# Kernel optimization log

Hardware: AMD Instinct MI355X
Metric: run time of the kernel (lower is better)

Reference implementation:

```python
import jax, jax.numpy as jnp
import numpy as np
import math

EMBED_DIM = 1024
NUM_HEADS = 16
HEAD_DIM = EMBED_DIM // NUM_HEADS
D_FF = 4 * EMBED_DIM
EPS = 1e-6  # flax LayerNorm default


def _layer_norm(x, scale, bias):
    mu = jnp.mean(x, axis=-1, keepdims=True)
    var = jnp.mean(jnp.square(x - mu), axis=-1, keepdims=True)
    return (x - mu) * jax.lax.rsqrt(var + EPS) * scale + bias


def setup_inputs() -> dict:
    key = jax.random.key(0)
    ks = jax.random.split(key, 12)
    B, T, D = 8, 1024, EMBED_DIM
    x = jax.random.normal(ks[0], (B, T, D), dtype=jnp.float32)
    # causal mask broadcastable to [B, H, T, T]
    mask = jnp.tril(jnp.ones((T, T), dtype=bool))[None, None, :, :]
    mask = jnp.broadcast_to(mask, (B, 1, T, T))
    s = 0.02
    return {
        "x": x,
        "mask": mask,
        "ln1_scale": jnp.ones((D,), jnp.float32),
        "ln1_bias": jnp.zeros((D,), jnp.float32),
        "wq": jax.random.normal(ks[1], (D, D), jnp.float32) * s,
        "bq": jnp.zeros((D,), jnp.float32),
        "wk": jax.random.normal(ks[2], (D, D), jnp.float32) * s,
        "bk": jnp.zeros((D,), jnp.float32),
        "wv": jax.random.normal(ks[3], (D, D), jnp.float32) * s,
        "bv": jnp.zeros((D,), jnp.float32),
        "wo": jax.random.normal(ks[4], (D, D), jnp.float32) * s,
        "bo": jnp.zeros((D,), jnp.float32),
        "ln2_scale": jnp.ones((D,), jnp.float32),
        "ln2_bias": jnp.zeros((D,), jnp.float32),
        "w1": jax.random.normal(ks[5], (D, D_FF), jnp.float32) * s,
        "b1": jnp.zeros((D_FF,), jnp.float32),
        "w2": jax.random.normal(ks[6], (D_FF, D), jnp.float32) * s,
        "b2": jnp.zeros((D,), jnp.float32),
    }


def reference(x, mask, ln1_scale, ln1_bias, wq, bq, wk, bk, wv, bv, wo, bo,
              ln2_scale, ln2_bias, w1, b1, w2, b2):
    B, T, D = x.shape
    residual = x
    h = _layer_norm(x, ln1_scale, ln1_bias)
    q = (h @ wq + bq).reshape(B, T, NUM_HEADS, HEAD_DIM)
    k = (h @ wk + bk).reshape(B, T, NUM_HEADS, HEAD_DIM)
    v = (h @ wv + bv).reshape(B, T, NUM_HEADS, HEAD_DIM)
    # scores: [B, H, T, T]
    scores = jnp.einsum("bqhd,bkhd->bhqk", q, k) / math.sqrt(HEAD_DIM)
    scores = jnp.where(mask, scores, -1e9)
    probs = jax.nn.softmax(scores, axis=-1)
    # dropout is identity (deterministic=True)
    out = jnp.einsum("bhqk,bkhd->bqhd", probs, v).reshape(B, T, D)
    h = out @ wo + bo
    x = h + residual
    residual = x
    h = _layer_norm(x, ln2_scale, ln2_bias)
    h = jax.nn.gelu(h @ w1 + b1, approximate=True)  # flax nn.gelu default
    h = h @ w2 + b2
    return h + residual
```

## Files before the change

kernel.cpp:

```cpp
#include <hip/hip_runtime.h>
#include <hip/hip_bf16.h>

using bf16 = __hip_bfloat16;
typedef __attribute__((ext_vector_type(8))) short bf16x8;
typedef __attribute__((ext_vector_type(4))) float f32x4;

__device__ inline float u2f(unsigned int u) { return __uint_as_float(u << 16); }
__device__ inline float toF(float x) { return x; }
__device__ inline float toF(bf16 x) { return __bfloat162float(x); }
__device__ inline void storeO(float* p, float v) { *p = v; }
__device__ inline void storeO(bf16* p, float v) { *p = __float2bfloat16(v); }

__device__ inline void gload_lds16(const void* g, void* l) {
    __builtin_amdgcn_global_load_lds(
        (const __attribute__((address_space(1))) void*)g,
        (__attribute__((address_space(3))) void*)l, 16, 0, 0);
}

__device__ inline void wgbar() {
    asm volatile("s_waitcnt lgkmcnt(0)" ::: "memory");
    __builtin_amdgcn_s_barrier();
    asm volatile("" ::: "memory");
}

__device__ inline int swzb(int row, int bcol) {
    return row * 128 + (bcol ^ (((row ^ (row >> 3)) & 7) << 4));
}

__global__ __launch_bounds__(256) void transpose_k(const float* __restrict__ in,
                                                   bf16* __restrict__ out,
                                                   int R, int C) {
    __shared__ float tile[32][33];
    const int c0 = blockIdx.x * 32, r0 = blockIdx.y * 32;
    const int tx = threadIdx.x & 31, ty = threadIdx.x >> 5;
#pragma unroll
    for (int i = 0; i < 32; i += 8)
        tile[ty + i][tx] = in[(size_t)(r0 + ty + i) * C + (c0 + tx)];
    __syncthreads();
#pragma unroll
    for (int i = 0; i < 32; i += 8)
        out[(size_t)(c0 + ty + i) * R + (r0 + tx)] = __float2bfloat16(tile[tx][ty + i]);
}

__global__ __launch_bounds__(256) void catb_k(const float* __restrict__ a,
                                              const float* __restrict__ b,
                                              const float* __restrict__ c,
                                              float* __restrict__ o) {
    const int t = blockIdx.x * 256 + threadIdx.x;
    const float* s = t < 1024 ? a : (t < 2048 ? b : c);
    o[t] = s[t & 1023];
}

__device__ inline float waveRedSum(float x) {
#pragma unroll
    for (int off = 32; off; off >>= 1) x += __shfl_xor(x, off, 64);
    return x;
}

template <typename T>
__global__ __launch_bounds__(256) void layernorm_k(const T* __restrict__ in,
                                                   const float* __restrict__ g,
                                                   const float* __restrict__ bta,
                                                   bf16* __restrict__ out) {
    const int row = blockIdx.x, t = threadIdx.x;
    const int lane = t & 63, wid = t >> 6;
    const T* xr = in + (size_t)row * 1024;
    float v0, v1, v2, v3;
    if constexpr (sizeof(T) == 4) {
        float4 u = ((const float4*)xr)[t];
        v0 = u.x; v1 = u.y; v2 = u.z; v3 = u.w;
    } else {
        ushort4 u = ((const ushort4*)xr)[t];
        v0 = u2f(u.x); v1 = u2f(u.y); v2 = u2f(u.z); v3 = u2f(u.w);
    }
    __shared__ float red[8];
    float s = waveRedSum(v0 + v1 + v2 + v3);
    if (lane == 0) red[wid] = s;
    __syncthreads();
    float mu = (red[0] + red[1] + red[2] + red[3]) * (1.f / 1024.f);
    float d0 = v0 - mu, d1 = v1 - mu, d2 = v2 - mu, d3 = v3 - mu;
    float ss = waveRedSum(d0 * d0 + d1 * d1 + d2 * d2 + d3 * d3);
    if (lane == 0) red[4 + wid] = ss;
    __syncthreads();
    float var = (red[4] + red[5] + red[6] + red[7]) * (1.f / 1024.f);
    float inv = rsqrtf(var + 1e-6f);
    const int c = t * 4;
    bf16* orow = out + (size_t)row * 1024;
    orow[c + 0] = __float2bfloat16(d0 * inv * g[c + 0] + bta[c + 0]);
    orow[c + 1] = __float2bfloat16(d1 * inv * g[c + 1] + bta[c + 1]);
    orow[c + 2] = __float2bfloat16(d2 * inv * g[c + 2] + bta[c + 2]);
    orow[c + 3] = __float2bfloat16(d3 * inv * g[c + 3] + bta[c + 3]);
}

template <int GELU, int RES, int ACC, typename RT, typename OT>
__global__ __launch_bounds__(256) void mgemm_k(const bf16* __restrict__ A,
                                               const bf16* __restrict__ B, int ldB,
                                               const float* __restrict__ bias,
                                               const RT* __restrict__ resid,
                                               OT* C, int M, int N, int K, int gx) {
    __shared__ bf16 As[2 * 128 * 32];
    __shared__ bf16 Bs[2 * 128 * 32];
    const int tid = threadIdx.x;
    const int lane = tid & 63, wid = tid >> 6;
    const int l16 = lane & 15, quad = lane >> 4;
    const int wm = (wid >> 1) * 64, wn = (wid & 1) * 64;
    const int nwg = gridDim.x;
    const int wg = ((blockIdx.x & 7) * (nwg >> 3)) + (blockIdx.x >> 3);
    const int m0 = (wg / gx) * 128, n0 = (wg % gx) * 128;

    const int r0 = tid >> 2, sc0 = tid & 3;
    const int lc0 = sc0 ^ ((r0 >> 1) & 3);
    const int r1 = r0 + 64;
    const int lc1 = sc0 ^ ((r1 >> 1) & 3);
    const bf16* gA0 = A + (size_t)(m0 + r0) * K + lc0 * 8;
    const bf16* gA1 = A + (size_t)(m0 + r1) * K + lc1 * 8;
    const bf16* gB0 = B + (size_t)(n0 + r0) * ldB + lc0 * 8;
    const bf16* gB1 = B + (size_t)(n0 + r1) * ldB + lc1 * 8;
    char* asb = (char*)As;
    char* bsb = (char*)Bs;
    const int lb0 = wid * 1024, lb1 = 4096 + wid * 1024;
    const int rdsw = (quad ^ ((l16 >> 1) & 3)) * 16;

    f32x4 acc[4][4] = {};
    const int nT = K >> 5;
    gload_lds16(gA0, asb + lb0);
    gload_lds16(gA1, asb + lb1);
    gload_lds16(gB0, bsb + lb0);
    gload_lds16(gB1, bsb + lb1);
    __syncthreads();
    for (int t = 0; t < nT; ++t) {
        const int cur = t & 1;
        if (t + 1 < nT) {
            char* ab = asb + (cur ^ 1) * 8192;
            char* bb = bsb + (cur ^ 1) * 8192;
            const int ko = (t + 1) * 32;
            gload_lds16(gA0 + ko, ab + lb0);
            gload_lds16(gA1 + ko, ab + lb1);
            gload_lds16(gB0 + ko, bb + lb0);
            gload_lds16(gB1 + ko, bb + lb1);
        }
        const char* ar = asb + cur * 8192;
        const char* br = bsb + cur * 8192;
        bf16x8 a[4], b[4];
#pragma unroll
        for (int i = 0; i < 4; ++i)
            a[i] = *(const bf16x8*)(ar + (wm + i * 16 + l16) * 64 + rdsw);
#pragma unroll
        for (int i = 0; i < 4; ++i)
            b[i] = *(const bf16x8*)(br + (wn + i * 16 + l16) * 64 + rdsw);
        __builtin_amdgcn_s_setprio(1);
#pragma unroll
        for (int mi = 0; mi < 4; ++mi)
#pragma unroll
            for (int ni = 0; ni < 4; ++ni)
                acc[mi][ni] = __builtin_amdgcn_mfma_f32_16x16x32_bf16(
                    a[mi], b[ni], acc[mi][ni], 0, 0, 0);
        __builtin_amdgcn_s_setprio(0);
        __syncthreads();
    }
#pragma unroll
    for (int mi = 0; mi < 4; ++mi) {
#pragma unroll
        for (int ni = 0; ni < 4; ++ni) {
            const int col = n0 + wn + ni * 16 + l16;
            const float bv = bias ? bias[col] : 0.f;
#pragma unroll
            for (int r = 0; r < 4; ++r) {
                const int row = m0 + wm + mi * 16 + quad * 4 + r;
                float val = acc[mi][ni][r] + bv;
                if (GELU) {
                    float z = 0.7978845608028654f * (val + 0.044715f * val * val * val);
                    float th = 1.f - 2.f / (__expf(2.f * z) + 1.f);
                    val = 0.5f * val * (1.f + th);
                }
                const size_t idx = (size_t)row * N + col;
                if (RES) val += toF(resid[idx]);
                if (ACC) val += toF(C[idx]);
                storeO(&C[idx], val);
            }
        }
    }
}

__global__ __launch_bounds__(256) void attn_k(const bf16* __restrict__ q,
                                              const bf16* __restrict__ k,
                                              const bf16* __restrict__ v,
                                              bf16* __restrict__ o, int rs) {
    const int bid = blockIdx.x;
    const int u = bid & 255, top = bid >> 8;
    const int xx = u & 3;
    const int h = (u >> 2) & 15;
    const int b = top * 4 + (u >> 6);
    const int qi = top ? 3 - xx : xx;
    const int qblock = qi * 256;
    const int tid = threadIdx.x;
    const int wave = tid >> 6, lane = tid & 63;
    const int l16 = lane & 15, quad = lane >> 4;
    const int q0w = qblock + wave * 64;

    __shared__ __align__(16) bf16 Kl[64 * 64];
    __shared__ __align__(16) bf16 Vt[64 * 64];
    __shared__ __align__(16) bf16 Pl[4 * 64 * 64];
    __shared__ __align__(16) float sc[4][64];

    bf16x8 qf[4][2];
#pragma unroll
    for (int ni = 0; ni < 4; ++ni) {
        const int row = q0w + ni * 16 + l16;
        const bf16* qp = q + ((size_t)b * 1024 + row) * rs + h * 64;
#pragma unroll
        for (int kc = 0; kc < 2; ++kc)
            qf[ni][kc] = *(const bf16x8*)(qp + kc * 32 + quad * 8);
    }

    f32x4 acc[4][4] = {};
    float mrun[4], lrun[4];
#pragma unroll
    for (int ni = 0; ni < 4; ++ni) { mrun[ni] = -1e30f; lrun[ni] = 0.f; }

    const int NT = qi * 4 + 4;
    const int myNT = qi * 4 + wave + 1;

    const int kr_ = tid >> 3, kch = tid & 7;
    const int vr_ = (tid >> 3) * 2, vdb = (tid & 7) * 8;
    uint4 kA, kB, vA, vB;
    {
        const size_t gk = ((size_t)b * 1024 + 0 + kr_) * rs + h * 64 + kch * 8;
        kA = *(const uint4*)(k + gk);
        kB = *(const uint4*)(k + gk + (size_t)32 * rs);
        const size_t gv = ((size_t)b * 1024 + 0 + vr_) * rs + h * 64 + vdb;
        vA = *(const uint4*)(v + gv);
        vB = *(const uint4*)(v + gv + rs);
    }

    for (int t = 0; t < NT; ++t) {
        wgbar();
        *(uint4*)((char*)Kl + swzb(kr_, kch * 16)) = kA;
        *(uint4*)((char*)Kl + swzb(kr_ + 32, kch * 16)) = kB;
        {
            const unsigned aw[4] = {vA.x, vA.y, vA.z, vA.w};
            const unsigned bw[4] = {vB.x, vB.y, vB.z, vB.w};
#pragma unroll
            for (int j = 0; j < 8; ++j) {
                const unsigned lo = (aw[j >> 1] >> ((j & 1) * 16)) & 0xffffu;
                const unsigned hi = (bw[j >> 1] >> ((j & 1) * 16)) & 0xffffu;
                *(unsigned*)((char*)Vt + swzb(vdb + j, vr_ * 2)) = lo | (hi << 16);
            }
        }
        if (t + 1 < NT) {
            const int j1 = (t + 1) * 64;
            const size_t gk = ((size_t)b * 1024 + j1 + kr_) * rs + h * 64 + kch * 8;
            kA = *(const uint4*)(k + gk);
            kB = *(const uint4*)(k + gk + (size_t)32 * rs);
            const size_t gv = ((size_t)b * 1024 + j1 + vr_) * rs + h * 64 + vdb;
            vA = *(const uint4*)(v + gv);
            vB = *(const uint4*)(v + gv + rs);
        }
        wgbar();
        if (t < myNT) {
            const int j0 = t * 64;
            f32x4 st[4][4] = {};
#pragma unroll
            for (int kc = 0; kc < 2; ++kc) {
                bf16x8 kf[4];
#pragma unroll
                for (int mi = 0; mi < 4; ++mi)
                    kf[mi] = *(const bf16x8*)((char*)Kl +
                             swzb(mi * 16 + l16, kc * 64 + quad * 16));
                __builtin_amdgcn_s_setprio(1);
#pragma unroll
                for (int mi = 0; mi < 4; ++mi)
#pragma unroll
                    for (int ni = 0; ni < 4; ++ni)
                        st[mi][ni] = __builtin_amdgcn_mfma_f32_16x16x32_bf16(
                            kf[mi], qf[ni][kc], st[mi][ni], 0, 0, 0);
                __builtin_amdgcn_s_setprio(0);
            }
            if (j0 == q0w) {
#pragma unroll
                for (int mi = 0; mi < 4; ++mi)
#pragma unroll
                    for (int ni = 0; ni < 4; ++ni)
#pragma unroll
                        for (int r = 0; r < 4; ++r)
                            if (mi * 16 + quad * 4 + r > ni * 16 + l16)
                                st[mi][ni][r] = -1e30f;
            }
            float mx[4];
#pragma unroll
            for (int ni = 0; ni < 4; ++ni) {
                float a0 = fmaxf(st[0][ni][0], st[0][ni][1]);
                float a1 = fmaxf(st[0][ni][2], st[0][ni][3]);
                float a2 = fmaxf(st[1][ni][0], st[1][ni][1]);
                float a3 = fmaxf(st[1][ni][2], st[1][ni][3]);
                float a4 = fmaxf(st[2][ni][0], st[2][ni][1]);
                float a5 = fmaxf(st[2][ni][2], st[2][ni][3]);
                float a6 = fmaxf(st[3][ni][0], st[3][ni][1]);
                float a7 = fmaxf(st[3][ni][2], st[3][ni][3]);
                float m_ = fmaxf(fmaxf(fmaxf(a0, a1), fmaxf(a2, a3)),
                                 fmaxf(fmaxf(a4, a5), fmaxf(a6, a7)));
                m_ = fmaxf(m_, __shfl_xor(m_, 16, 64));
                m_ = fmaxf(m_, __shfl_xor(m_, 32, 64));
                mx[ni] = m_;
            }
            const bool need = (mx[0] > mrun[0] + 64.f) | (mx[1] > mrun[1] + 64.f) |
                              (mx[2] > mrun[2] + 64.f) | (mx[3] > mrun[3] + 64.f);
            if (__any(need)) {
                float fac[4];
#pragma unroll
                for (int ni = 0; ni < 4; ++ni) {
                    const float nm = (mx[ni] > mrun[ni] + 64.f) ? mx[ni] : mrun[ni];
                    fac[ni] = __expf((mrun[ni] - nm) * 0.125f);
                    mrun[ni] = nm;
                    lrun[ni] *= fac[ni];
                }
                if (quad == 0)
#pragma unroll
                    for (int ni = 0; ni < 4; ++ni) sc[wave][ni * 16 + l16] = fac[ni];
#pragma unroll
                for (int mi = 0; mi < 4; ++mi) {
                    const f32x4 f4 = *(const f32x4*)&sc[wave][mi * 16 + quad * 4];
#pragma unroll
                    for (int ni = 0; ni < 4; ++ni)
#pragma unroll
                        for (int r = 0; r < 4; ++r) acc[mi][ni][r] *= f4[r];
                }
            }
#pragma unroll
            for (int ni = 0; ni < 4; ++ni) {
                const float mm = mrun[ni];
                float t0 = 0.f, t1 = 0.f, t2 = 0.f, t3 = 0.f;
#pragma unroll
                for (int mi = 0; mi < 4; ++mi) {
                    float p0 = __expf((st[mi][ni][0] - mm) * 0.125f);
                    float p1 = __expf((st[mi][ni][1] - mm) * 0.125f);
                    float p2 = __expf((st[mi][ni][2] - mm) * 0.125f);
                    float p3 = __expf((st[mi][ni][3] - mm) * 0.125f);
                    st[mi][ni][0] = p0; st[mi][ni][1] = p1;
                    st[mi][ni][2] = p2; st[mi][ni][3] = p3;
                    t0 += p0; t1 += p1; t2 += p2; t3 += p3;
                }
                float ls = (t0 + t1) + (t2 + t3);
                ls += __shfl_xor(ls, 16, 64);
                ls += __shfl_xor(ls, 32, 64);
                lrun[ni] += ls;
            }
            char* Pb = (char*)Pl + wave * 8192;
#pragma unroll
            for (int ni = 0; ni < 4; ++ni) {
                const int qrow = ni * 16 + l16;
#pragma unroll
                for (int mi = 0; mi < 4; ++mi) {
                    union { bf16 bv[4]; uint2 u2; } pk;
#pragma unroll
                    for (int r = 0; r < 4; ++r)
                        pk.bv[r] = __float2bfloat16(st[mi][ni][r]);
                    *(uint2*)(Pb + swzb(qrow, mi * 32 + quad * 8)) = pk.u2;
                }
            }
#pragma unroll
            for (int kc = 0; kc < 2; ++kc) {
                bf16x8 pf[4], vf[4];
#pragma unroll
                for (int mi = 0; mi < 4; ++mi)
                    pf[mi] = *(const bf16x8*)(Pb +
                             swzb(mi * 16 + l16, kc * 64 + quad * 16));
#pragma unroll
                for (int ni = 0; ni < 4; ++ni)
                    vf[ni] = *(const bf16x8*)((char*)Vt +
                             swzb(ni * 16 + l16, kc * 64 + quad * 16));
                __builtin_amdgcn_s_setprio(1);
#pragma unroll
                for (int mi = 0; mi < 4; ++mi)
#pragma unroll
                    for (int ni = 0; ni < 4; ++ni)
                        acc[mi][ni] = __builtin_amdgcn_mfma_f32_16x16x32_bf16(
                            pf[mi], vf[ni], acc[mi][ni], 0, 0, 0);
                __builtin_amdgcn_s_setprio(0);
            }
        }
    }
    if (quad == 0)
#pragma unroll
        for (int ni = 0; ni < 4; ++ni) sc[wave][ni * 16 + l16] = lrun[ni];
#pragma unroll
    for (int mi = 0; mi < 4; ++mi) {
        const f32x4 l4 = *(const f32x4*)&sc[wave][mi * 16 + quad * 4];
#pragma unroll
        for (int r = 0; r < 4; ++r) {
            const float inv = 1.f / l4[r];
            const int row = q0w + mi * 16 + quad * 4 + r;
            bf16* orow = o + ((size_t)b * 1024 + row) * 1024 + h * 64;
#pragma unroll
            for (int ni = 0; ni < 4; ++ni)
                orow[ni * 16 + l16] = __float2bfloat16(acc[mi][ni][r] * inv);
        }
    }
}

extern "C" void kernel_launch(void* const* d_in, const int* in_sizes, int n_in,
                              void* d_out, int out_size, void* d_ws, size_t ws_size,
                              hipStream_t stream) {
    (void)out_size; (void)ws_size;
    const float* x = (const float*)d_in[0];
    const int base = (n_in >= 18 && in_sizes[1] > 4096) ? 2 : 1;
    const float* ln1s = (const float*)d_in[base + 0];
    const float* ln1b = (const float*)d_in[base + 1];
    const float* wq   = (const float*)d_in[base + 2];
    const float* bq   = (const float*)d_in[base + 3];
    const float* wk   = (const float*)d_in[base + 4];
    const float* bk   = (const float*)d_in[base + 5];
    const float* wv   = (const float*)d_in[base + 6];
    const float* bv   = (const float*)d_in[base + 7];
    const float* wo   = (const float*)d_in[base + 8];
    const float* bo   = (const float*)d_in[base + 9];
    const float* ln2s = (const float*)d_in[base + 10];
    const float* ln2b = (const float*)d_in[base + 11];
    const float* w1   = (const float*)d_in[base + 12];
    const float* b1   = (const float*)d_in[base + 13];
    const float* w2   = (const float*)d_in[base + 14];
    const float* b2   = (const float*)d_in[base + 15];
    float* out = (float*)d_out;

    char* ws = (char*)d_ws;
    char* oc = (char*)d_out;
    const size_t MB = 1ull << 20;
    bf16* h     = (bf16*)(ws + 0 * MB);
    bf16* qkv   = (bf16*)(ws + 16 * MB);
    bf16* ao    = (bf16*)(ws + 0 * MB);
    bf16* h2    = (bf16*)(ws + 0 * MB);
    bf16* woT   = (bf16*)(ws + 16 * MB);
    bf16* f1c   = (bf16*)(ws + 16 * MB);
    bf16* w1T   = (bf16*)(ws + 48 * MB);
    bf16* w2T   = (bf16*)(ws + 56 * MB);
    bf16* wqkvT = (bf16*)(oc + 0 * MB);
    float* bqkv = (float*)(oc + 8 * MB);

    const dim3 tb(256);

    layernorm_k<float><<<8192, tb, 0, stream>>>(x, ln1s, ln1b, h);
    transpose_k<<<dim3(32, 32), tb, 0, stream>>>(wq, wqkvT, 1024, 1024);
    transpose_k<<<dim3(32, 32), tb, 0, stream>>>(wk, wqkvT + 1024 * 1024, 1024, 1024);
    transpose_k<<<dim3(32, 32), tb, 0, stream>>>(wv, wqkvT + 2 * 1024 * 1024, 1024, 1024);
    catb_k<<<12, tb, 0, stream>>>(bq, bk, bv, bqkv);
    mgemm_k<0, 0, 0, float, bf16><<<1536, tb, 0, stream>>>(
        h, wqkvT, 1024, bqkv, nullptr, qkv, 8192, 3072, 1024, 24);
    attn_k<<<512, tb, 0, stream>>>(qkv, qkv + 1024, qkv + 2048, ao, 3072);
    transpose_k<<<dim3(32, 32), tb, 0, stream>>>(wo, woT, 1024, 1024);
    transpose_k<<<dim3(128, 32), tb, 0, stream>>>(w1, w1T, 1024, 4096);
    transpose_k<<<dim3(32, 128), tb, 0, stream>>>(w2, w2T, 4096, 1024);
    mgemm_k<0, 1, 0, float, float><<<512, tb, 0, stream>>>(
        ao, woT, 1024, bo, x, out, 8192, 1024, 1024, 8);
    layernorm_k<float><<<8192, tb, 0, stream>>>(out, ln2s, ln2b, h2);
    for (int c = 0; c < 2; ++c) {
        mgemm_k<1, 0, 0, float, bf16><<<1024, tb, 0, stream>>>(
            h2, w1T + (size_t)c * 2048 * 1024, 1024, b1 + c * 2048, nullptr,
            f1c, 8192, 2048, 1024, 16);
        mgemm_k<0, 0, 1, float, float><<<512, tb, 0, stream>>>(
            f1c, w2T + c * 2048, 4096, c ? nullptr : b2, nullptr,
            out, 8192, 1024, 2048, 8);
    }
}
```

Before: 584.3 us.

## Triple-buffer GEMM loads and add 256x256 tile kernel for QKV and FFN1

```diff
diff --git a/kernel.cpp b/kernel.cpp
--- a/kernel.cpp
+++ b/kernel.cpp
@@ -98,8 +98,8 @@
                                                const float* __restrict__ bias,
                                                const RT* __restrict__ resid,
                                                OT* C, int M, int N, int K, int gx) {
-    __shared__ bf16 As[2 * 128 * 32];
-    __shared__ bf16 Bs[2 * 128 * 32];
+    __shared__ bf16 As[3 * 128 * 32];
+    __shared__ bf16 Bs[3 * 128 * 32];
     const int tid = threadIdx.x;
     const int lane = tid & 63, wid = tid >> 6;
     const int l16 = lane & 15, quad = lane >> 4;
@@ -123,24 +123,35 @@
 
     f32x4 acc[4][4] = {};
     const int nT = K >> 5;
-    gload_lds16(gA0, asb + lb0);
-    gload_lds16(gA1, asb + lb1);
-    gload_lds16(gB0, bsb + lb0);
-    gload_lds16(gB1, bsb + lb1);
-    __syncthreads();
+#pragma unroll
+    for (int p = 0; p < 2; ++p) {
+        char* ab = asb + p * 8192;
+        char* bb = bsb + p * 8192;
+        const int ko = p * 32;
+        gload_lds16(gA0 + ko, ab + lb0);
+        gload_lds16(gA1 + ko, ab + lb1);
+        gload_lds16(gB0 + ko, bb + lb0);
+        gload_lds16(gB1 + ko, bb + lb1);
+    }
+    int issued = 2;
     for (int t = 0; t < nT; ++t) {
-        const int cur = t & 1;
-        if (t + 1 < nT) {
-            char* ab = asb + (cur ^ 1) * 8192;
-            char* bb = bsb + (cur ^ 1) * 8192;
-            const int ko = (t + 1) * 32;
+        if (issued > t + 1)
+            asm volatile("s_waitcnt vmcnt(4)" ::: "memory");
+        else
+            asm volatile("s_waitcnt vmcnt(0)" ::: "memory");
+        __builtin_amdgcn_s_barrier();
+        if (issued < nT) {
+            char* ab = asb + (issued % 3) * 8192;
+            char* bb = bsb + (issued % 3) * 8192;
+            const int ko = issued * 32;
             gload_lds16(gA0 + ko, ab + lb0);
             gload_lds16(gA1 + ko, ab + lb1);
             gload_lds16(gB0 + ko, bb + lb0);
             gload_lds16(gB1 + ko, bb + lb1);
-        }
-        const char* ar = asb + cur * 8192;
-        const char* br = bsb + cur * 8192;
+            ++issued;
+        }
+        const char* ar = asb + (t % 3) * 8192;
+        const char* br = bsb + (t % 3) * 8192;
         bf16x8 a[4], b[4];
 #pragma unroll
         for (int i = 0; i < 4; ++i)
@@ -156,7 +167,6 @@
                 acc[mi][ni] = __builtin_amdgcn_mfma_f32_16x16x32_bf16(
                     a[mi], b[ni], acc[mi][ni], 0, 0, 0);
         __builtin_amdgcn_s_setprio(0);
-        __syncthreads();
     }
 #pragma unroll
     for (int mi = 0; mi < 4; ++mi) {
@@ -177,6 +187,103 @@
                 if (RES) val += toF(resid[idx]);
                 if (ACC) val += toF(C[idx]);
                 storeO(&C[idx], val);
+            }
+        }
+    }
+}
+
+template <int GELU>
+__global__ __launch_bounds__(512, 2) void gemm256_k(const bf16* __restrict__ A,
+                                                    const bf16* __restrict__ B, int ldB,
+                                                    const float* __restrict__ bias,
+                                                    bf16* __restrict__ C,
+                                                    int M, int N, int K, int gx) {
+    __shared__ bf16 As[3 * 256 * 32];
+    __shared__ bf16 Bs[3 * 256 * 32];
+    const int tid = threadIdx.x;
+    const int lane = tid & 63, wid = tid >> 6;
+    const int l16 = lane & 15, quad = lane >> 4;
+    const int wm = (wid >> 2) * 128, wn = (wid & 3) * 64;
+    const int nwg = gridDim.x;
+    const int wg = ((blockIdx.x & 7) * (nwg >> 3)) + (blockIdx.x >> 3);
+    const int m0 = (wg / gx) * 256, n0 = (wg % gx) * 256;
+
+    const int r0 = tid >> 2, sc0 = tid & 3;
+    const int lc0 = sc0 ^ ((r0 >> 1) & 3);
+    const int r1 = r0 + 128;
+    const int lc1 = sc0 ^ ((r1 >> 1) & 3);
+    const bf16* gA0 = A + (size_t)(m0 + r0) * K + lc0 * 8;
+    const bf16* gA1 = A + (size_t)(m0 + r1) * K + lc1 * 8;
+    const bf16* gB0 = B + (size_t)(n0 + r0) * ldB + lc0 * 8;
+    const bf16* gB1 = B + (size_t)(n0 + r1) * ldB + lc1 * 8;
+    char* asb = (char*)As;
+    char* bsb = (char*)Bs;
+    const int lb0 = wid * 1024, lb1 = 8192 + wid * 1024;
+    const int rdsw = (quad ^ ((l16 >> 1) & 3)) * 16;
+
+    f32x4 acc[8][4] = {};
+    const int nT = K >> 5;
+#pragma unroll
+    for (int p = 0; p < 2; ++p) {
+        char* ab = asb + p * 16384;
+        char* bb = bsb + p * 16384;
+        const int ko = p * 32;
+        gload_lds16(gA0 + ko, ab + lb0);
+        gload_lds16(gA1 + ko, ab + lb1);
+        gload_lds16(gB0 + ko, bb + lb0);
+        gload_lds16(gB1 + ko, bb + lb1);
+    }
+    int issued = 2;
+    for (int t = 0; t < nT; ++t) {
+        if (issued > t + 1)
+            asm volatile("s_waitcnt vmcnt(4)" ::: "memory");
+        else
+            asm volatile("s_waitcnt vmcnt(0)" ::: "memory");
+        __builtin_amdgcn_s_barrier();
+        if (issued < nT) {
+            char* ab = asb + (issued % 3) * 16384;
+            char* bb = bsb + (issued % 3) * 16384;
+            const int ko = issued * 32;
+            gload_lds16(gA0 + ko, ab + lb0);
+            gload_lds16(gA1 + ko, ab + lb1);
+            gload_lds16(gB0 + ko, bb + lb0);
+            gload_lds16(gB1 + ko, bb + lb1);
+            ++issued;
+        }
+        const char* ar = asb + (t % 3) * 16384;
+        const char* br = bsb + (t % 3) * 16384;
+        bf16x8 a[8], b[4];
+#pragma unroll
+        for (int i = 0; i < 8; ++i)
+            a[i] = *(const bf16x8*)(ar + (wm + i * 16 + l16) * 64 + rdsw);
+#pragma unroll
+        for (int i = 0; i < 4; ++i)
+            b[i] = *(const bf16x8*)(br + (wn + i * 16 + l16) * 64 + rdsw);
+        __builtin_amdgcn_s_setprio(1);
+#pragma unroll
+        for (int mi = 0; mi < 8; ++mi)
+#pragma unroll
+            for (int ni = 0; ni < 4; ++ni)
+                acc[mi][ni] = __builtin_amdgcn_mfma_f32_16x16x32_bf16(
+                    a[mi], b[ni], acc[mi][ni], 0, 0, 0);
+        __builtin_amdgcn_s_setprio(0);
+    }
+#pragma unroll
+    for (int mi = 0; mi < 8; ++mi) {
+#pragma unroll
+        for (int ni = 0; ni < 4; ++ni) {
+            const int col = n0 + wn + ni * 16 + l16;
+            const float bv = bias[col];
+#pragma unroll
+            for (int r = 0; r < 4; ++r) {
+                const int row = m0 + wm + mi * 16 + quad * 4 + r;
+                float val = acc[mi][ni][r] + bv;
+                if (GELU) {
+                    float z = 0.7978845608028654f * (val + 0.044715f * val * val * val);
+                    float th = 1.f - 2.f / (__expf(2.f * z) + 1.f);
+                    val = 0.5f * val * (1.f + th);
+                }
+                C[(size_t)row * N + col] = __float2bfloat16(val);
             }
         }
     }
@@ -443,8 +550,8 @@
     transpose_k<<<dim3(32, 32), tb, 0, stream>>>(wk, wqkvT + 1024 * 1024, 1024, 1024);
     transpose_k<<<dim3(32, 32), tb, 0, stream>>>(wv, wqkvT + 2 * 1024 * 1024, 1024, 1024);
     catb_k<<<12, tb, 0, stream>>>(bq, bk, bv, bqkv);
-    mgemm_k<0, 0, 0, float, bf16><<<1536, tb, 0, stream>>>(
-        h, wqkvT, 1024, bqkv, nullptr, qkv, 8192, 3072, 1024, 24);
+    gemm256_k<0><<<384, 512, 0, stream>>>(
+        h, wqkvT, 1024, bqkv, qkv, 8192, 3072, 1024, 12);
     attn_k<<<512, tb, 0, stream>>>(qkv, qkv + 1024, qkv + 2048, ao, 3072);
     transpose_k<<<dim3(32, 32), tb, 0, stream>>>(wo, woT, 1024, 1024);
     transpose_k<<<dim3(128, 32), tb, 0, stream>>>(w1, w1T, 1024, 4096);
@@ -453,9 +560,9 @@
         ao, woT, 1024, bo, x, out, 8192, 1024, 1024, 8);
     layernorm_k<float><<<8192, tb, 0, stream>>>(out, ln2s, ln2b, h2);
     for (int c = 0; c < 2; ++c) {
-        mgemm_k<1, 0, 0, float, bf16><<<1024, tb, 0, stream>>>(
-            h2, w1T + (size_t)c * 2048 * 1024, 1024, b1 + c * 2048, nullptr,
-            f1c, 8192, 2048, 1024, 16);
+        gemm256_k<1><<<256, 512, 0, stream>>>(
+            h2, w1T + (size_t)c * 2048 * 1024, 1024, b1 + c * 2048,
+            f1c, 8192, 2048, 1024, 8);
         mgemm_k<0, 0, 1, float, float><<<512, tb, 0, stream>>>(
             f1c, w2T + c * 2048, 4096, c ? nullptr : b2, nullptr,
             out, 8192, 1024, 2048, 8);
```

After: 602.3 us. 3.1% more time.

## Triple-buffer GEMM LDS loads with vmcnt waits and merge QKV weight transposes

Applied to the files above, without the earlier changes.

```diff
diff --git a/kernel.cpp b/kernel.cpp
--- a/kernel.cpp
+++ b/kernel.cpp
@@ -40,6 +40,24 @@
 #pragma unroll
     for (int i = 0; i < 32; i += 8)
         out[(size_t)(c0 + ty + i) * R + (r0 + tx)] = __float2bfloat16(tile[tx][ty + i]);
+}
+
+__global__ __launch_bounds__(256) void qkvT_k(const float* __restrict__ wq,
+                                              const float* __restrict__ wk,
+                                              const float* __restrict__ wv,
+                                              bf16* __restrict__ out) {
+    __shared__ float tile[32][33];
+    const float* in = blockIdx.z == 0 ? wq : (blockIdx.z == 1 ? wk : wv);
+    bf16* o = out + (size_t)blockIdx.z * 1024 * 1024;
+    const int c0 = blockIdx.x * 32, r0 = blockIdx.y * 32;
+    const int tx = threadIdx.x & 31, ty = threadIdx.x >> 5;
+#pragma unroll
+    for (int i = 0; i < 32; i += 8)
+        tile[ty + i][tx] = in[(size_t)(r0 + ty + i) * 1024 + (c0 + tx)];
+    __syncthreads();
+#pragma unroll
+    for (int i = 0; i < 32; i += 8)
+        o[(size_t)(c0 + ty + i) * 1024 + (r0 + tx)] = __float2bfloat16(tile[tx][ty + i]);
 }
 
 __global__ __launch_bounds__(256) void catb_k(const float* __restrict__ a,
@@ -98,8 +116,8 @@
                                                const float* __restrict__ bias,
                                                const RT* __restrict__ resid,
                                                OT* C, int M, int N, int K, int gx) {
-    __shared__ bf16 As[2 * 128 * 32];
-    __shared__ bf16 Bs[2 * 128 * 32];
+    __shared__ bf16 As[3 * 128 * 32];
+    __shared__ bf16 Bs[3 * 128 * 32];
     const int tid = threadIdx.x;
     const int lane = tid & 63, wid = tid >> 6;
     const int l16 = lane & 15, quad = lane >> 4;
@@ -123,24 +141,35 @@
 
     f32x4 acc[4][4] = {};
     const int nT = K >> 5;
-    gload_lds16(gA0, asb + lb0);
-    gload_lds16(gA1, asb + lb1);
-    gload_lds16(gB0, bsb + lb0);
-    gload_lds16(gB1, bsb + lb1);
-    __syncthreads();
+#pragma unroll
+    for (int p = 0; p < 2; ++p) {
+        char* ab = asb + p * 8192;
+        char* bb = bsb + p * 8192;
+        const int ko = p * 32;
+        gload_lds16(gA0 + ko, ab + lb0);
+        gload_lds16(gA1 + ko, ab + lb1);
+        gload_lds16(gB0 + ko, bb + lb0);
+        gload_lds16(gB1 + ko, bb + lb1);
+    }
+    int issued = 2;
     for (int t = 0; t < nT; ++t) {
-        const int cur = t & 1;
-        if (t + 1 < nT) {
-            char* ab = asb + (cur ^ 1) * 8192;
-            char* bb = bsb + (cur ^ 1) * 8192;
-            const int ko = (t + 1) * 32;
+        if (issued > t + 1)
+            asm volatile("s_waitcnt vmcnt(4)" ::: "memory");
+        else
+            asm volatile("s_waitcnt vmcnt(0)" ::: "memory");
+        __builtin_amdgcn_s_barrier();
+        if (issued < nT) {
+            char* ab = asb + (issued % 3) * 8192;
+            char* bb = bsb + (issued % 3) * 8192;
+            const int ko = issued * 32;
             gload_lds16(gA0 + ko, ab + lb0);
             gload_lds16(gA1 + ko, ab + lb1);
             gload_lds16(gB0 + ko, bb + lb0);
             gload_lds16(gB1 + ko, bb + lb1);
-        }
-        const char* ar = asb + cur * 8192;
-        const char* br = bsb + cur * 8192;
+            ++issued;
+        }
+        const char* ar = asb + (t % 3) * 8192;
+        const char* br = bsb + (t % 3) * 8192;
         bf16x8 a[4], b[4];
 #pragma unroll
         for (int i = 0; i < 4; ++i)
@@ -156,7 +185,6 @@
                 acc[mi][ni] = __builtin_amdgcn_mfma_f32_16x16x32_bf16(
                     a[mi], b[ni], acc[mi][ni], 0, 0, 0);
         __builtin_amdgcn_s_setprio(0);
-        __syncthreads();
     }
 #pragma unroll
     for (int mi = 0; mi < 4; ++mi) {
@@ -439,9 +467,7 @@
     const dim3 tb(256);
 
     layernorm_k<float><<<8192, tb, 0, stream>>>(x, ln1s, ln1b, h);
-    transpose_k<<<dim3(32, 32), tb, 0, stream>>>(wq, wqkvT, 1024, 1024);
-    transpose_k<<<dim3(32, 32), tb, 0, stream>>>(wk, wqkvT + 1024 * 1024, 1024, 1024);
-    transpose_k<<<dim3(32, 32), tb, 0, stream>>>(wv, wqkvT + 2 * 1024 * 1024, 1024, 1024);
+    qkvT_k<<<dim3(32, 32, 3), tb, 0, stream>>>(wq, wk, wv, wqkvT);
     catb_k<<<12, tb, 0, stream>>>(bq, bk, bv, bqkv);
     mgemm_k<0, 0, 0, float, bf16><<<1536, tb, 0, stream>>>(
         h, wqkvT, 1024, bqkv, nullptr, qkv, 8192, 3072, 1024, 24);
```

New measurement: 597.1 us. 2.2% more time.
